# Kernel optimization log

Hardware: AMD Instinct MI355X
Metric: run time of the kernel (lower is better)

## Reference

```python
import jax, jax.numpy as jnp
import numpy as np

# --- problem-size constants (uniform instance of the ragged structure) ---
B = 64            # claims
EVI = 5           # evidence sequences per claim
SEQS = B * EVI    # total PLM sequences
L = 256           # tokens per sequence
D = 768           # in_channels (PLM hidden)
WORDS = 32        # word-nodes per evidence
TPW = 4           # token refs averaged per word (word_select mean)
N = B * EVI * WORDS   # total graph nodes = 10240
E = N * 16            # edges
R = 4                 # num_relations
DOUT = 768            # out_channels
LH = 1024             # linear_hidden_channels
NC = 3                # num_class


def setup_inputs() -> dict:
    key = jax.random.key(0)
    ks = jax.random.split(key, 16)
    s = 0.02
    return {
        "token_feats": jax.random.normal(ks[0], (SEQS, L, D), jnp.float32),
        "concat_cls": jax.random.normal(ks[1], (B, D), jnp.float32),
        "W_rel1": jax.random.normal(ks[2], (R, D, D), jnp.float32) * s,
        "W_root1": jax.random.normal(ks[3], (D, D), jnp.float32) * s,
        "b1": jnp.zeros((D,), jnp.float32),
        "W_rel2": jax.random.normal(ks[4], (R, D, DOUT), jnp.float32) * s,
        "W_root2": jax.random.normal(ks[5], (D, DOUT), jnp.float32) * s,
        "b2": jnp.zeros((DOUT,), jnp.float32),
        "att_w0": jax.random.normal(ks[6], (D + 2 * DOUT, DOUT), jnp.float32) * s,
        "att_w1": jax.random.normal(ks[7], (DOUT, 1), jnp.float32) * s,
        "lin1_w": jax.random.normal(ks[8], (2 * DOUT + D, LH), jnp.float32) * s,
        "lin1_b": jnp.zeros((LH,), jnp.float32),
        "lin2_w": jax.random.normal(ks[9], (LH, NC), jnp.float32) * s,
        "lin2_b": jnp.zeros((NC,), jnp.float32),
        "word_token_idx": jax.random.randint(ks[10], (N * TPW,), 0, SEQS * L),
        "edge_index": jax.random.randint(ks[11], (2, E), 0, N),
        "edge_type": jax.random.randint(ks[12], (E,), 0, R),
        "claim_seq_idx": jnp.arange(B) * EVI,  # first sequence of each claim
    }


def _rgcn(x, edge_index, edge_type, W_rel, W_root, b):
    # PyG RGCNConv with mean aggregation per relation + root transform + bias
    xr = jnp.einsum('nd,rde->rne', x, W_rel)        # [R, N, Dout]
    src, dst = edge_index[0], edge_index[1]
    msg = xr[edge_type, src]                        # [E, Dout]
    seg = dst * R + edge_type                       # (target, relation) buckets
    cnt = jax.ops.segment_sum(jnp.ones((E,), x.dtype), seg, num_segments=N * R)
    msg = msg / jnp.maximum(cnt, 1.0)[seg][:, None]
    agg = jax.ops.segment_sum(msg, dst, num_segments=N)
    return agg + x @ W_root + b


def reference(token_feats, concat_cls, W_rel1, W_root1, b1, W_rel2, W_root2, b2,
              att_w0, att_w1, lin1_w, lin1_b, lin2_w, lin2_b,
              word_token_idx, edge_index, edge_type, claim_seq_idx):
    # word_select: mean of token vectors per word-node (TPW uniform here)
    tok = token_feats.reshape(-1, D)
    x = tok[word_token_idx].reshape(N, TPW, D).mean(axis=1)       # [N, D]
    claim_cls = token_feats[claim_seq_idx, 0, :]                  # [B, D]

    # 2 RGCN layers with ReLU
    x = jax.nn.relu(_rgcn(x, edge_index, edge_type, W_rel1, W_root1, b1))
    x = jax.nn.relu(_rgcn(x, edge_index, edge_type, W_rel2, W_root2, b2))

    # per-evidence mean||max pooling over its words (uniform WORDS per evidence)
    xe = x.reshape(B * EVI, WORDS, DOUT)
    ev = jnp.concatenate([xe.mean(axis=1), xe.max(axis=1)], axis=-1)  # [B*EVI, 2*Dout]

    # attention scores per evidence, conditioned on the claim CLS
    cc = jnp.repeat(claim_cls, EVI, axis=0)                       # [B*EVI, D]
    h = jax.nn.relu(jnp.concatenate([cc, ev], axis=-1) @ att_w0)
    p = h @ att_w1                                                # [B*EVI, 1]

    # per-claim softmax over its evidences, weighted sum of evidence reps
    a = jax.nn.softmax(p.reshape(B, EVI), axis=1)
    graph = jnp.einsum('be,bed->bd', a, ev.reshape(B, EVI, 2 * DOUT))  # [B, 2*Dout]

    rep = jnp.concatenate([graph, concat_cls], axis=-1)           # [B, 2*Dout + D]
    # dropout is identity in eval mode
    out = jax.nn.log_softmax(jax.nn.relu(rep @ lin1_w + lin1_b) @ lin2_w + lin2_b, axis=-1)
    attention = jax.nn.sigmoid(p[:, 0])                           # [B*EVI]
    return out, attention
```

## Files before the change

### kernel.cpp

```cpp
#include <hip/hip_runtime.h>
#include <hip/hip_fp16.h>


#define BN 64
#define EVI 5
#define SEQS (BN * EVI)
#define LSEQ 256
#define DIM 768
#define WORDS 32
#define TPW 4
#define NNODE (BN * EVI * WORDS)
#define NEDGE (NNODE * 16)
#define RREL 4
#define DOUT 768
#define LH 1024
#define NCLS 3
#define KBIG (5 * DIM)
#define KATT (DIM + 2 * DOUT)

typedef float f32x4 __attribute__((ext_vector_type(4)));
typedef __bf16 bf16x8 __attribute__((ext_vector_type(8)));

__device__ inline unsigned short f2bf(float f) {
    union { float f; unsigned int u; } v; v.f = f;
    unsigned int u = v.u;
    unsigned int lsb = (u >> 16) & 1u;
    u += 0x7fffu + lsb;
    return (unsigned short)(u >> 16);
}
__device__ inline float bf2f(unsigned short h) {
    union { float f; unsigned int u; } v; v.u = ((unsigned int)h) << 16; return v.f;
}

__device__ inline float ldin(const void* p, long i, int f) {
    if (f == 1) return __half2float(((const __half*)p)[i]);
    if (f == 2) return bf2f(((const unsigned short*)p)[i]);
    return ((const float*)p)[i];
}

__global__ void detect_kernel(const void* w, int* flag) {
    if (blockIdx.x != 0) return;
    const int lane = threadIdx.x;
    const unsigned int* u32 = (const unsigned int*)w;
    const unsigned short* u16 = (const unsigned short*)w;
    int tiny = 0;
    for (int i = lane; i < 2048; i += 64) {
        unsigned int b = u32[i];
        float f; __builtin_memcpy(&f, &b, 4);
        float a = fabsf(f);
        if (!(a > 1e-10f)) tiny++;
    }
    int band = 0;
    for (int i = lane; i < 4096; i += 64) {
        unsigned short h = u16[i];
        int e8 = (h >> 7) & 0xFF;
        if (h == 0 || (e8 >= 0x66 && e8 <= 0x86)) band++;
    }
#pragma unroll
    for (int o = 32; o > 0; o >>= 1) {
        tiny += __shfl_down(tiny, o);
        band += __shfl_down(band, o);
    }
    if (lane == 0) {
        if (tiny > 1024) { *flag = 1; return; }
        *flag = (band > 3900) ? 2 : 0;
    }
}

__global__ void convert_kernel(const void* __restrict__ src, float* __restrict__ dst,
                               long n, const int* __restrict__ flag)
{
    int f = *flag;
    long stride = (long)gridDim.x * 256;
    for (long i = (long)blockIdx.x * 256 + threadIdx.x; i < n; i += stride)
        dst[i] = ldin(src, i, f);
}

__global__ __launch_bounds__(256) void gather_mean_kernel(
    const void* __restrict__ tok, const int* __restrict__ widx,
    unsigned short* __restrict__ xb, const int* __restrict__ flag)
{
    int f = *flag;
    int n = blockIdx.x;
    long i0 = widx[n * 4 + 0], i1 = widx[n * 4 + 1];
    long i2 = widx[n * 4 + 2], i3 = widx[n * 4 + 3];
    for (int c = threadIdx.x; c < DIM; c += 256) {
        float s = ldin(tok, i0 * DIM + c, f) + ldin(tok, i1 * DIM + c, f)
                + ldin(tok, i2 * DIM + c, f) + ldin(tok, i3 * DIM + c, f);
        xb[(long)n * DIM + c] = f2bf(s * 0.25f);
    }
}

__global__ void count_kernel(const int* __restrict__ ei, const int* __restrict__ et,
                             int* __restrict__ cnt)
{
    int e = blockIdx.x * 256 + threadIdx.x;
    if (e >= NEDGE) return;
    int dst = ei[NEDGE + e];
    int r = et[e];
    atomicAdd(&cnt[dst * RREL + r], 1);
}

__global__ __launch_bounds__(1024) void scan_kernel(const int* __restrict__ cnt,
                                                    int* __restrict__ offs, int n)
{
    __shared__ int buf[1024];
    __shared__ int carry;
    int tid = threadIdx.x;
    if (tid == 0) { carry = 0; offs[0] = 0; }
    __syncthreads();
    for (int base = 0; base < n; base += 1024) {
        int v = (base + tid < n) ? cnt[base + tid] : 0;
        buf[tid] = v;
        __syncthreads();
        for (int o = 1; o < 1024; o <<= 1) {
            int t = (tid >= o) ? buf[tid - o] : 0;
            __syncthreads();
            buf[tid] += t;
            __syncthreads();
        }
        if (base + tid < n) offs[base + tid + 1] = carry + buf[tid];
        __syncthreads();
        if (tid == 0) carry += buf[1023];
        __syncthreads();
    }
}

__global__ void fill_kernel(const int* __restrict__ ei, const int* __restrict__ et,
                            const int* __restrict__ offs, int* __restrict__ cursor,
                            int* __restrict__ sorted)
{
    int e = blockIdx.x * 256 + threadIdx.x;
    if (e >= NEDGE) return;
    int src = ei[e];
    int dst = ei[NEDGE + e];
    int r = et[e];
    int seg = dst * RREL + r;
    int pos = offs[seg] + atomicAdd(&cursor[seg], 1);
    sorted[pos] = src;
}

__global__ __launch_bounds__(256) void aggregate_kernel(
    const unsigned short* __restrict__ xsrc, long xstride,
    const int* __restrict__ offs, const int* __restrict__ sorted,
    unsigned short* __restrict__ A, int write_root)
{
    int n = blockIdx.x;
    long base = (long)n * KBIG;
    for (int r = 0; r < RREL; r++) {
        int s0 = offs[n * RREL + r], s1 = offs[n * RREL + r + 1];
        float inv = 1.0f / (float)max(s1 - s0, 1);
        for (int c = threadIdx.x; c < DIM; c += 256) {
            float acc = 0.0f;
            for (int i = s0; i < s1; i++) {
                long s = sorted[i];
                acc += bf2f(xsrc[s * xstride + c]);
            }
            A[base + r * DIM + c] = f2bf(acc * inv);
        }
    }
    if (write_root) {
        for (int c = threadIdx.x; c < DIM; c += 256)
            A[base + 4 * DIM + c] = xsrc[(long)n * xstride + c];
    }
}

__global__ __launch_bounds__(256) void transpose_cast_kernel(
    const float* __restrict__ in, int Ncols,
    unsigned short* __restrict__ out, int outStride, int colOff)
{
    __shared__ float t[32][33];
    int kt = blockIdx.x * 32, nt = blockIdx.y * 32;
    int lx = threadIdx.x & 31, ly = threadIdx.x >> 5;
    for (int i = 0; i < 4; i++)
        t[ly + i * 8][lx] = in[(long)(kt + ly + i * 8) * Ncols + nt + lx];
    __syncthreads();
    for (int i = 0; i < 4; i++)
        out[(long)(nt + ly + i * 8) * outStride + colOff + kt + lx] = f2bf(t[lx][ly + i * 8]);
}

__global__ __launch_bounds__(256) void gemm_bt_kernel(
    const unsigned short* __restrict__ A, const unsigned short* __restrict__ Bt,
    int K, const float* __restrict__ bias, int relu,
    float* __restrict__ outF, long strideF,
    unsigned short* __restrict__ outB, long strideB)
{
    __shared__ __align__(16) unsigned short As[128 * 32];
    __shared__ __align__(16) unsigned short Bs[128 * 32];
    const int tid = threadIdx.x;
    const int lane = tid & 63, wv = tid >> 6;
    const int wr = wv >> 1, wc = wv & 1;
    const int lr = lane & 15, q = lane >> 4;
    const long m0 = (long)blockIdx.x * 128, n0 = (long)blockIdx.y * 128;

    f32x4 acc[4][4] = {};

    for (int kt = 0; kt < K; kt += 32) {
#pragma unroll
        for (int i = 0; i < 2; i++) {
            int chunk = i * 256 + tid;
            int row = chunk >> 2, kc = (chunk & 3) * 8;
            const unsigned short* ga = A + (m0 + row) * K + kt + kc;
            const unsigned short* gb = Bt + (n0 + row) * K + kt + kc;
            int ldsbase = (i * 256 + wv * 64) * 8;
            __builtin_amdgcn_global_load_lds(
                (const __attribute__((address_space(1))) void*)ga,
                (__attribute__((address_space(3))) void*)&As[ldsbase], 16, 0, 0);
            __builtin_amdgcn_global_load_lds(
                (const __attribute__((address_space(1))) void*)gb,
                (__attribute__((address_space(3))) void*)&Bs[ldsbase], 16, 0, 0);
        }
        __syncthreads();
        bf16x8 af[4], bfr[4];
#pragma unroll
        for (int i = 0; i < 4; i++)
            af[i] = *(const bf16x8*)&As[(wr * 64 + i * 16 + lr) * 32 + q * 8];
#pragma unroll
        for (int j = 0; j < 4; j++)
            bfr[j] = *(const bf16x8*)&Bs[(wc * 64 + j * 16 + lr) * 32 + q * 8];
#pragma unroll
        for (int i = 0; i < 4; i++)
#pragma unroll
            for (int j = 0; j < 4; j++)
                acc[i][j] = __builtin_amdgcn_mfma_f32_16x16x32_bf16(af[i], bfr[j], acc[i][j], 0, 0, 0);
        __syncthreads();
    }

#pragma unroll
    for (int i = 0; i < 4; i++) {
#pragma unroll
        for (int j = 0; j < 4; j++) {
            long col = n0 + wc * 64 + j * 16 + lr;
            float bv = bias ? bias[col] : 0.0f;
#pragma unroll
            for (int r = 0; r < 4; r++) {
                long row = m0 + wr * 64 + i * 16 + q * 4 + r;
                float v = acc[i][j][r] + bv;
                if (relu) v = fmaxf(v, 0.0f);
                if (outF) outF[row * strideF + col] = v;
                if (outB) outB[row * strideB + col] = f2bf(v);
            }
        }
    }
}

__global__ __launch_bounds__(256) void pool_cc_kernel(
    const float* __restrict__ C2, const void* __restrict__ tok,
    const int* __restrict__ csi, unsigned short* __restrict__ A3,
    float* __restrict__ evF, const int* __restrict__ flag)
{
    int f = *flag;
    int s = blockIdx.x;
    int b = s / EVI;
    long seq = csi[b];
    for (int c = threadIdx.x; c < DIM; c += 256) {
        float mx = -1e30f, sm = 0.0f;
        const float* col = C2 + (long)s * WORDS * DOUT + c;
        for (int w = 0; w < WORDS; w++) {
            float v = col[(long)w * DOUT];
            sm += v;
            mx = fmaxf(mx, v);
        }
        float mean = sm * (1.0f / WORDS);
        evF[(long)s * (2 * DOUT) + c] = mean;
        evF[(long)s * (2 * DOUT) + DOUT + c] = mx;
        A3[(long)s * KATT + c] = f2bf(ldin(tok, seq * LSEQ * DIM + c, f));
        A3[(long)s * KATT + DIM + c] = f2bf(mean);
        A3[(long)s * KATT + DIM + DOUT + c] = f2bf(mx);
    }
}

__global__ __launch_bounds__(256) void pdot_kernel(
    const float* __restrict__ h, const float* __restrict__ w1, float* __restrict__ p)
{
    int i = blockIdx.x;
    float s = 0.0f;
    for (int k = threadIdx.x; k < DOUT; k += 256) s += h[(long)i * DOUT + k] * w1[k];
    __shared__ float red[256];
    red[threadIdx.x] = s;
    __syncthreads();
    for (int o = 128; o > 0; o >>= 1) {
        if (threadIdx.x < o) red[threadIdx.x] += red[threadIdx.x + o];
        __syncthreads();
    }
    if (threadIdx.x == 0) p[i] = red[0];
}

__global__ void att_out_kernel(const float* __restrict__ p, float* __restrict__ out)
{
    int i = blockIdx.x * 256 + threadIdx.x;
    if (i < SEQS) out[BN * NCLS + i] = 1.0f / (1.0f + __expf(-p[i]));
}

__global__ __launch_bounds__(256) void softgraph_kernel(
    const float* __restrict__ p, const float* __restrict__ evF,
    const float* __restrict__ ccls, unsigned short* __restrict__ A4)
{
    int b = blockIdx.x;
    __shared__ float a[EVI];
    if (threadIdx.x == 0) {
        float m = -1e30f;
        for (int e = 0; e < EVI; e++) m = fmaxf(m, p[b * EVI + e]);
        float s = 0.0f, ex[EVI];
        for (int e = 0; e < EVI; e++) { ex[e] = __expf(p[b * EVI + e] - m); s += ex[e]; }
        for (int e = 0; e < EVI; e++) a[e] = ex[e] / s;
    }
    __syncthreads();
    for (int d = threadIdx.x; d < 2 * DOUT; d += 256) {
        float g = 0.0f;
        for (int e = 0; e < EVI; e++)
            g += a[e] * evF[(long)(b * EVI + e) * (2 * DOUT) + d];
        A4[(long)b * KATT + d] = f2bf(g);
    }
    for (int c = threadIdx.x; c < DIM; c += 256)
        A4[(long)b * KATT + 2 * DOUT + c] = f2bf(ccls[(long)b * DIM + c]);
}

__global__ __launch_bounds__(256) void final_kernel(
    const float* __restrict__ C4, const float* __restrict__ w2,
    const float* __restrict__ bb, float* __restrict__ out)
{
    int b = blockIdx.x;
    float s0 = 0.0f, s1 = 0.0f, s2 = 0.0f;
    for (int k = threadIdx.x; k < LH; k += 256) {
        float h = C4[(long)b * LH + k];
        s0 += h * w2[k * NCLS + 0];
        s1 += h * w2[k * NCLS + 1];
        s2 += h * w2[k * NCLS + 2];
    }
    __shared__ float r0[256], r1[256], r2[256];
    int t = threadIdx.x;
    r0[t] = s0; r1[t] = s1; r2[t] = s2;
    __syncthreads();
    for (int o = 128; o > 0; o >>= 1) {
        if (t < o) { r0[t] += r0[t + o]; r1[t] += r1[t + o]; r2[t] += r2[t + o]; }
        __syncthreads();
    }
    if (t == 0) {
        float l0 = r0[0] + bb[0], l1 = r1[0] + bb[1], l2 = r2[0] + bb[2];
        float m = fmaxf(l0, fmaxf(l1, l2));
        float lse = logf(__expf(l0 - m) + __expf(l1 - m) + __expf(l2 - m)) + m;
        out[b * NCLS + 0] = l0 - lse;
        out[b * NCLS + 1] = l1 - lse;
        out[b * NCLS + 2] = l2 - lse;
    }
}

extern "C" void kernel_launch(void* const* d_in, const int* in_sizes, int n_in,
                              void* d_out, int out_size, void* d_ws, size_t ws_size,
                              hipStream_t stream)
{
    const void* tok      = d_in[0];
    const void* ccls_r   = d_in[1];
    const void* W_rel1_r = d_in[2];
    const void* W_root1_r= d_in[3];
    const void* b1_r     = d_in[4];
    const void* W_rel2_r = d_in[5];
    const void* W_root2_r= d_in[6];
    const void* b2_r     = d_in[7];
    const void* att_w0_r = d_in[8];
    const void* att_w1_r = d_in[9];
    const void* lin1_w_r = d_in[10];
    const void* lin1_b_r = d_in[11];
    const void* lin2_w_r = d_in[12];
    const void* lin2_b_r = d_in[13];
    const int* widx      = (const int*)d_in[14];
    const int* ei        = (const int*)d_in[15];
    const int* et        = (const int*)d_in[16];
    const int* csi       = (const int*)d_in[17];
    float* out           = (float*)d_out;

    char* ws = (char*)d_ws;
    size_t off = 0;
    auto alloc = [&](size_t bytes) { size_t o = off; off = (off + bytes + 255) & ~(size_t)255; return o; };

    int* flag   = (int*)(ws + alloc(256));
    float* cclsF   = (float*)(ws + alloc((size_t)BN * DIM * 4));
    float* Wrel1F  = (float*)(ws + alloc((size_t)RREL * DIM * DIM * 4));
    float* Wroot1F = (float*)(ws + alloc((size_t)DIM * DIM * 4));
    float* b1F     = (float*)(ws + alloc((size_t)DIM * 4));
    float* Wrel2F  = (float*)(ws + alloc((size_t)RREL * DIM * DOUT * 4));
    float* Wroot2F = (float*)(ws + alloc((size_t)DIM * DOUT * 4));
    float* b2F     = (float*)(ws + alloc((size_t)DOUT * 4));
    float* aw0F    = (float*)(ws + alloc((size_t)KATT * DOUT * 4));
    float* aw1F    = (float*)(ws + alloc((size_t)DOUT * 4));
    float* l1wF    = (float*)(ws + alloc((size_t)KATT * LH * 4));
    float* l1bF    = (float*)(ws + alloc((size_t)LH * 4));
    float* l2wF    = (float*)(ws + alloc((size_t)LH * NCLS * 4));
    float* l2bF    = (float*)(ws + alloc((size_t)NCLS * 4));
    unsigned short* xb  = (unsigned short*)(ws + alloc((size_t)NNODE * DIM * 2));
    unsigned short* A1  = (unsigned short*)(ws + alloc((size_t)NNODE * KBIG * 2));
    unsigned short* X1  = (unsigned short*)(ws + alloc((size_t)NNODE * DOUT * 2));
    unsigned short* Wt1 = (unsigned short*)(ws + alloc((size_t)DIM * KBIG * 2));
    unsigned short* Wt2 = (unsigned short*)(ws + alloc((size_t)DIM * KBIG * 2));
    unsigned short* Wt3 = (unsigned short*)(ws + alloc((size_t)DOUT * KATT * 2));
    unsigned short* Wt4 = (unsigned short*)(ws + alloc((size_t)LH * KATT * 2));
    float* C2           = (float*)(ws + alloc((size_t)NNODE * DOUT * 4));
    unsigned short* A3  = (unsigned short*)(ws + alloc((size_t)384 * KATT * 2));
    float* C3           = (float*)(ws + alloc((size_t)384 * DOUT * 4));
    float* evF          = (float*)(ws + alloc((size_t)SEQS * 2 * DOUT * 4));
    float* pbuf         = (float*)(ws + alloc((size_t)SEQS * 4));
    unsigned short* A4  = (unsigned short*)(ws + alloc((size_t)128 * KATT * 2));
    float* C4           = (float*)(ws + alloc((size_t)128 * LH * 4));
    int* cnt            = (int*)(ws + alloc((size_t)2 * NNODE * RREL * 4));
    int* cursor         = cnt + NNODE * RREL;
    int* offs           = (int*)(ws + alloc((size_t)(NNODE * RREL + 1) * 4));
    int* sorted         = (int*)(ws + alloc((size_t)NEDGE * 4));
    (void)ws_size; (void)in_sizes; (void)n_in; (void)out_size;

    detect_kernel<<<1, 64, 0, stream>>>(W_rel1_r, flag);
    auto conv = [&](const void* src, float* dst, long n) {
        int grid = (int)min((n + 255) / 256, (long)2048);
        convert_kernel<<<grid, 256, 0, stream>>>(src, dst, n, flag);
    };
    conv(ccls_r,   cclsF,   (long)BN * DIM);
    conv(W_rel1_r, Wrel1F,  (long)RREL * DIM * DIM);
    conv(W_root1_r,Wroot1F, (long)DIM * DIM);
    conv(b1_r,     b1F,     DIM);
    conv(W_rel2_r, Wrel2F,  (long)RREL * DIM * DOUT);
    conv(W_root2_r,Wroot2F, (long)DIM * DOUT);
    conv(b2_r,     b2F,     DOUT);
    conv(att_w0_r, aw0F,    (long)KATT * DOUT);
    conv(att_w1_r, aw1F,    DOUT);
    conv(lin1_w_r, l1wF,    (long)KATT * LH);
    conv(lin1_b_r, l1bF,    LH);
    conv(lin2_w_r, l2wF,    (long)LH * NCLS);
    conv(lin2_b_r, l2bF,    NCLS);

    hipMemsetAsync(cnt, 0, (size_t)2 * NNODE * RREL * 4, stream);
    count_kernel<<<NEDGE / 256, 256, 0, stream>>>(ei, et, cnt);
    scan_kernel<<<1, 1024, 0, stream>>>(cnt, offs, NNODE * RREL);
    fill_kernel<<<NEDGE / 256, 256, 0, stream>>>(ei, et, offs, cursor, sorted);

    gather_mean_kernel<<<NNODE, 256, 0, stream>>>(tok, widx, xb, flag);

    transpose_cast_kernel<<<dim3(96, 24), 256, 0, stream>>>(Wrel1F, DIM, Wt1, KBIG, 0);
    transpose_cast_kernel<<<dim3(24, 24), 256, 0, stream>>>(Wroot1F, DIM, Wt1, KBIG, 4 * DIM);
    transpose_cast_kernel<<<dim3(96, 24), 256, 0, stream>>>(Wrel2F, DOUT, Wt2, KBIG, 0);
    transpose_cast_kernel<<<dim3(24, 24), 256, 0, stream>>>(Wroot2F, DOUT, Wt2, KBIG, 4 * DIM);
    transpose_cast_kernel<<<dim3(72, 24), 256, 0, stream>>>(aw0F, DOUT, Wt3, KATT, 0);
    transpose_cast_kernel<<<dim3(72, 32), 256, 0, stream>>>(l1wF, LH, Wt4, KATT, 0);

    aggregate_kernel<<<NNODE, 256, 0, stream>>>(xb, DIM, offs, sorted, A1, 1);
    gemm_bt_kernel<<<dim3(NNODE / 128, DIM / 128), 256, 0, stream>>>(
        A1, Wt1, KBIG, b1F, 1, nullptr, 0, X1, DOUT);

    aggregate_kernel<<<NNODE, 256, 0, stream>>>(X1, DOUT, offs, sorted, A1, 1);
    gemm_bt_kernel<<<dim3(NNODE / 128, DOUT / 128), 256, 0, stream>>>(
        A1, Wt2, KBIG, b2F, 1, C2, DOUT, nullptr, 0);

    pool_cc_kernel<<<SEQS, 256, 0, stream>>>(C2, tok, csi, A3, evF, flag);
    gemm_bt_kernel<<<dim3(3, DOUT / 128), 256, 0, stream>>>(
        A3, Wt3, KATT, nullptr, 1, C3, DOUT, nullptr, 0);
    pdot_kernel<<<SEQS, 256, 0, stream>>>(C3, aw1F, pbuf);
    att_out_kernel<<<(SEQS + 255) / 256, 256, 0, stream>>>(pbuf, out);
    softgraph_kernel<<<BN, 256, 0, stream>>>(pbuf, evF, cclsF, A4);

    gemm_bt_kernel<<<dim3(1, LH / 128), 256, 0, stream>>>(
        A4, Wt4, KATT, l1bF, 1, C4, LH, nullptr, 0);
    final_kernel<<<BN, 256, 0, stream>>>(C4, l2wF, l2bF, out);
}
```

Measured before the change: 1.072 ms.

## Fuse input dtype conversion into consumers and parallelize offset scan

Drops the separate fp32 conversion passes over the large weight matrices and classifier inputs. The transpose-cast, pdot, softgraph and final kernels now read the raw inputs directly through the dtype flag, which removes intermediate buffers and extra global traffic and launches. Separately, the single-block scan now gives each thread a contiguous chunk, scans the per-thread sums once, then writes local prefix sums, instead of looping over many 1024-element passes full of barriers. This adds a flag load and a dtype branch to each consumer kernel.

After: 1.058 ms. No clear change (-1.3%).

```diff
diff --git a/kernel.cpp b/kernel.cpp
--- a/kernel.cpp
+++ b/kernel.cpp
@@ -39,7 +39,6 @@
 }
 
 __global__ void detect_kernel(const void* w, int* flag) {
-    if (blockIdx.x != 0) return;
     const int lane = threadIdx.x;
     const unsigned int* u32 = (const unsigned int*)w;
     const unsigned short* u16 = (const unsigned short*)w;
@@ -104,25 +103,28 @@
 __global__ __launch_bounds__(1024) void scan_kernel(const int* __restrict__ cnt,
                                                     int* __restrict__ offs, int n)
 {
+    const int CH = (n + 1023) >> 10;
+    int tid = threadIdx.x;
+    int base = tid * CH;
+    int s = 0;
+    for (int i = 0; i < CH; i++)
+        if (base + i < n) s += cnt[base + i];
     __shared__ int buf[1024];
-    __shared__ int carry;
-    int tid = threadIdx.x;
-    if (tid == 0) { carry = 0; offs[0] = 0; }
+    buf[tid] = s;
     __syncthreads();
-    for (int base = 0; base < n; base += 1024) {
-        int v = (base + tid < n) ? cnt[base + tid] : 0;
-        buf[tid] = v;
-        __syncthreads();
-        for (int o = 1; o < 1024; o <<= 1) {
-            int t = (tid >= o) ? buf[tid - o] : 0;
-            __syncthreads();
-            buf[tid] += t;
-            __syncthreads();
+    for (int o = 1; o < 1024; o <<= 1) {
+        int t = (tid >= o) ? buf[tid - o] : 0;
+        __syncthreads();
+        buf[tid] += t;
+        __syncthreads();
+    }
+    int run = (tid == 0) ? 0 : buf[tid - 1];
+    if (tid == 0) offs[0] = 0;
+    for (int i = 0; i < CH; i++) {
+        if (base + i < n) {
+            run += cnt[base + i];
+            offs[base + i + 1] = run;
         }
-        if (base + tid < n) offs[base + tid + 1] = carry + buf[tid];
-        __syncthreads();
-        if (tid == 0) carry += buf[1023];
-        __syncthreads();
     }
 }
 
@@ -166,14 +168,16 @@
 }
 
 __global__ __launch_bounds__(256) void transpose_cast_kernel(
-    const float* __restrict__ in, int Ncols,
-    unsigned short* __restrict__ out, int outStride, int colOff)
-{
+    const void* __restrict__ in, int Ncols,
+    unsigned short* __restrict__ out, int outStride, int colOff,
+    const int* __restrict__ flag)
+{
+    int f = *flag;
     __shared__ float t[32][33];
     int kt = blockIdx.x * 32, nt = blockIdx.y * 32;
     int lx = threadIdx.x & 31, ly = threadIdx.x >> 5;
     for (int i = 0; i < 4; i++)
-        t[ly + i * 8][lx] = in[(long)(kt + ly + i * 8) * Ncols + nt + lx];
+        t[ly + i * 8][lx] = ldin(in, (long)(kt + ly + i * 8) * Ncols + nt + lx, f);
     __syncthreads();
     for (int i = 0; i < 4; i++)
         out[(long)(nt + ly + i * 8) * outStride + colOff + kt + lx] = f2bf(t[lx][ly + i * 8]);
@@ -271,11 +275,13 @@
 }
 
 __global__ __launch_bounds__(256) void pdot_kernel(
-    const float* __restrict__ h, const float* __restrict__ w1, float* __restrict__ p)
-{
+    const float* __restrict__ h, const void* __restrict__ w1, float* __restrict__ p,
+    const int* __restrict__ flag)
+{
+    int f = *flag;
     int i = blockIdx.x;
     float s = 0.0f;
-    for (int k = threadIdx.x; k < DOUT; k += 256) s += h[(long)i * DOUT + k] * w1[k];
+    for (int k = threadIdx.x; k < DOUT; k += 256) s += h[(long)i * DOUT + k] * ldin(w1, k, f);
     __shared__ float red[256];
     red[threadIdx.x] = s;
     __syncthreads();
@@ -294,8 +300,10 @@
 
 __global__ __launch_bounds__(256) void softgraph_kernel(
     const float* __restrict__ p, const float* __restrict__ evF,
-    const float* __restrict__ ccls, unsigned short* __restrict__ A4)
-{
+    const void* __restrict__ ccls, unsigned short* __restrict__ A4,
+    const int* __restrict__ flag)
+{
+    int f = *flag;
     int b = blockIdx.x;
     __shared__ float a[EVI];
     if (threadIdx.x == 0) {
@@ -313,20 +321,22 @@
         A4[(long)b * KATT + d] = f2bf(g);
     }
     for (int c = threadIdx.x; c < DIM; c += 256)
-        A4[(long)b * KATT + 2 * DOUT + c] = f2bf(ccls[(long)b * DIM + c]);
+        A4[(long)b * KATT + 2 * DOUT + c] = f2bf(ldin(ccls, (long)b * DIM + c, f));
 }
 
 __global__ __launch_bounds__(256) void final_kernel(
-    const float* __restrict__ C4, const float* __restrict__ w2,
-    const float* __restrict__ bb, float* __restrict__ out)
-{
+    const float* __restrict__ C4, const void* __restrict__ w2,
+    const void* __restrict__ bb, float* __restrict__ out,
+    const int* __restrict__ flag)
+{
+    int f = *flag;
     int b = blockIdx.x;
     float s0 = 0.0f, s1 = 0.0f, s2 = 0.0f;
     for (int k = threadIdx.x; k < LH; k += 256) {
         float h = C4[(long)b * LH + k];
-        s0 += h * w2[k * NCLS + 0];
-        s1 += h * w2[k * NCLS + 1];
-        s2 += h * w2[k * NCLS + 2];
+        s0 += h * ldin(w2, k * NCLS + 0, f);
+        s1 += h * ldin(w2, k * NCLS + 1, f);
+        s2 += h * ldin(w2, k * NCLS + 2, f);
     }
     __shared__ float r0[256], r1[256], r2[256];
     int t = threadIdx.x;
@@ -337,7 +347,7 @@
         __syncthreads();
     }
     if (t == 0) {
-        float l0 = r0[0] + bb[0], l1 = r1[0] + bb[1], l2 = r2[0] + bb[2];
+        float l0 = r0[0] + ldin(bb, 0, f), l1 = r1[0] + ldin(bb, 1, f), l2 = r2[0] + ldin(bb, 2, f);
         float m = fmaxf(l0, fmaxf(l1, l2));
         float lse = logf(__expf(l0 - m) + __expf(l1 - m) + __expf(l2 - m)) + m;
         out[b * NCLS + 0] = l0 - lse;
@@ -375,19 +385,9 @@
     auto alloc = [&](size_t bytes) { size_t o = off; off = (off + bytes + 255) & ~(size_t)255; return o; };
 
     int* flag   = (int*)(ws + alloc(256));
-    float* cclsF   = (float*)(ws + alloc((size_t)BN * DIM * 4));
-    float* Wrel1F  = (float*)(ws + alloc((size_t)RREL * DIM * DIM * 4));
-    float* Wroot1F = (float*)(ws + alloc((size_t)DIM * DIM * 4));
     float* b1F     = (float*)(ws + alloc((size_t)DIM * 4));
-    float* Wrel2F  = (float*)(ws + alloc((size_t)RREL * DIM * DOUT * 4));
-    float* Wroot2F = (float*)(ws + alloc((size_t)DIM * DOUT * 4));
     float* b2F     = (float*)(ws + alloc((size_t)DOUT * 4));
-    float* aw0F    = (float*)(ws + alloc((size_t)KATT * DOUT * 4));
-    float* aw1F    = (float*)(ws + alloc((size_t)DOUT * 4));
-    float* l1wF    = (float*)(ws + alloc((size_t)KATT * LH * 4));
     float* l1bF    = (float*)(ws + alloc((size_t)LH * 4));
-    float* l2wF    = (float*)(ws + alloc((size_t)LH * NCLS * 4));
-    float* l2bF    = (float*)(ws + alloc((size_t)NCLS * 4));
     unsigned short* xb  = (unsigned short*)(ws + alloc((size_t)NNODE * DIM * 2));
     unsigned short* A1  = (unsigned short*)(ws + alloc((size_t)NNODE * KBIG * 2));
     unsigned short* X1  = (unsigned short*)(ws + alloc((size_t)NNODE * DOUT * 2));
@@ -413,19 +413,9 @@
         int grid = (int)min((n + 255) / 256, (long)2048);
         convert_kernel<<<grid, 256, 0, stream>>>(src, dst, n, flag);
     };
-    conv(ccls_r,   cclsF,   (long)BN * DIM);
-    conv(W_rel1_r, Wrel1F,  (long)RREL * DIM * DIM);
-    conv(W_root1_r,Wroot1F, (long)DIM * DIM);
     conv(b1_r,     b1F,     DIM);
-    conv(W_rel2_r, Wrel2F,  (long)RREL * DIM * DOUT);
-    conv(W_root2_r,Wroot2F, (long)DIM * DOUT);
     conv(b2_r,     b2F,     DOUT);
-    conv(att_w0_r, aw0F,    (long)KATT * DOUT);
-    conv(att_w1_r, aw1F,    DOUT);
-    conv(lin1_w_r, l1wF,    (long)KATT * LH);
     conv(lin1_b_r, l1bF,    LH);
-    conv(lin2_w_r, l2wF,    (long)LH * NCLS);
-    conv(lin2_b_r, l2bF,    NCLS);
 
     hipMemsetAsync(cnt, 0, (size_t)2 * NNODE * RREL * 4, stream);
     count_kernel<<<NEDGE / 256, 256, 0, stream>>>(ei, et, cnt);
@@ -434,12 +424,12 @@
 
     gather_mean_kernel<<<NNODE, 256, 0, stream>>>(tok, widx, xb, flag);
 
-    transpose_cast_kernel<<<dim3(96, 24), 256, 0, stream>>>(Wrel1F, DIM, Wt1, KBIG, 0);
-    transpose_cast_kernel<<<dim3(24, 24), 256, 0, stream>>>(Wroot1F, DIM, Wt1, KBIG, 4 * DIM);
-    transpose_cast_kernel<<<dim3(96, 24), 256, 0, stream>>>(Wrel2F, DOUT, Wt2, KBIG, 0);
-    transpose_cast_kernel<<<dim3(24, 24), 256, 0, stream>>>(Wroot2F, DOUT, Wt2, KBIG, 4 * DIM);
-    transpose_cast_kernel<<<dim3(72, 24), 256, 0, stream>>>(aw0F, DOUT, Wt3, KATT, 0);
-    transpose_cast_kernel<<<dim3(72, 32), 256, 0, stream>>>(l1wF, LH, Wt4, KATT, 0);
+    transpose_cast_kernel<<<dim3(96, 24), 256, 0, stream>>>(W_rel1_r, DIM, Wt1, KBIG, 0, flag);
+    transpose_cast_kernel<<<dim3(24, 24), 256, 0, stream>>>(W_root1_r, DIM, Wt1, KBIG, 4 * DIM, flag);
+    transpose_cast_kernel<<<dim3(96, 24), 256, 0, stream>>>(W_rel2_r, DOUT, Wt2, KBIG, 0, flag);
+    transpose_cast_kernel<<<dim3(24, 24), 256, 0, stream>>>(W_root2_r, DOUT, Wt2, KBIG, 4 * DIM, flag);
+    transpose_cast_kernel<<<dim3(72, 24), 256, 0, stream>>>(att_w0_r, DOUT, Wt3, KATT, 0, flag);
+    transpose_cast_kernel<<<dim3(72, 32), 256, 0, stream>>>(lin1_w_r, LH, Wt4, KATT, 0, flag);
 
     aggregate_kernel<<<NNODE, 256, 0, stream>>>(xb, DIM, offs, sorted, A1, 1);
     gemm_bt_kernel<<<dim3(NNODE / 128, DIM / 128), 256, 0, stream>>>(
@@ -452,11 +442,11 @@
     pool_cc_kernel<<<SEQS, 256, 0, stream>>>(C2, tok, csi, A3, evF, flag);
     gemm_bt_kernel<<<dim3(3, DOUT / 128), 256, 0, stream>>>(
         A3, Wt3, KATT, nullptr, 1, C3, DOUT, nullptr, 0);
-    pdot_kernel<<<SEQS, 256, 0, stream>>>(C3, aw1F, pbuf);
+    pdot_kernel<<<SEQS, 256, 0, stream>>>(C3, att_w1_r, pbuf, flag);
     att_out_kernel<<<(SEQS + 255) / 256, 256, 0, stream>>>(pbuf, out);
-    softgraph_kernel<<<BN, 256, 0, stream>>>(pbuf, evF, cclsF, A4);
+    softgraph_kernel<<<BN, 256, 0, stream>>>(pbuf, evF, ccls_r, A4, flag);
 
     gemm_bt_kernel<<<dim3(1, LH / 128), 256, 0, stream>>>(
         A4, Wt4, KATT, l1bF, 1, C4, LH, nullptr, 0);
-    final_kernel<<<BN, 256, 0, stream>>>(C4, l2wF, l2bF, out);
-}
+    final_kernel<<<BN, 256, 0, stream>>>(C4, lin2_w_r, lin2_b_r, out, flag);
+}
```
